# Optimization experiments

Hardware: AMD Instinct MI355X
Metric: run time of the kernel (lower is better)

## Reference

```python
import jax, jax.numpy as jnp
import numpy as np

# Static graph layout: B equal-size graphs of N nodes; first S nodes of each
# graph are 'sentence' nodes, the remaining N-S are 'other' nodes.
B, N, S, C = 64, 4096, 512, 128
TOTAL = B * N
E = 4_194_304          # avg degree 16
K_SENT = 3             # num_output_sentences
RATIO = 0.5
K_OTHER = int(np.ceil(RATIO * (N - S)))  # 1792 -> 1795 kept nodes per graph


def setup_inputs() -> dict:
    key = jax.random.key(0)
    k1, k2, k3 = jax.random.split(key, 3)
    x = jax.random.normal(k1, (TOTAL, C), dtype=jnp.float32)
    weight = jax.random.uniform(k2, (C,), dtype=jnp.float32)  # torch.rand(1, C)
    edge_index = jax.random.randint(k3, (2, E), 0, TOTAL, dtype=jnp.int32)
    batch = jnp.repeat(jnp.arange(B, dtype=jnp.int32), N)     # per-node graph id
    return {"x": x, "weight": weight, "edge_index": edge_index, "batch": batch}


def _pool(x, weight, edge_index, batch):
    # score_i = tanh(<x_i, w> / ||w||)   (min_score is None branch)
    score = jnp.tanh((x @ weight) / jnp.linalg.norm(weight))        # [TOTAL]
    score_b = score.reshape(B, N)

    # ragged-as-dense per-graph top-k (torch does dense reshape + sort + gather)
    base = (jnp.arange(B, dtype=jnp.int32) * N)[:, None]            # [B,1]
    _, sent_idx = jax.lax.top_k(score_b[:, :S], K_SENT)             # [B,K_SENT]
    _, other_idx = jax.lax.top_k(score_b[:, S:], K_OTHER)           # [B,K_OTHER]
    perm = jnp.concatenate([
        (sent_idx.astype(jnp.int32) + base).reshape(-1),            # all sentence picks first
        (other_idx.astype(jnp.int32) + S + base).reshape(-1),
    ])                                                              # [B*(K_SENT+K_OTHER)]

    x_out = x[perm] * score[perm][:, None]                          # multiplier == 1
    batch_out = batch[perm]

    # filter_adj: remap kept nodes to new ids; drop edges touching dropped nodes.
    node_map = jnp.full((TOTAL,), -1, dtype=jnp.int32).at[perm].set(
        jnp.arange(perm.shape[0], dtype=jnp.int32))
    row = node_map[edge_index[0]]
    col = node_map[edge_index[1]]
    keep = (row >= 0) & (col >= 0)
    # jit-friendly compaction: stable-sort kept edges to the front, pad tail with -1
    order = jnp.argsort(jnp.where(keep, 0, 1), stable=True)
    edge_index_new = jnp.stack([jnp.where(keep, row, -1)[order],
                                jnp.where(keep, col, -1)[order]])
    num_edges = keep.sum()
    return x_out, edge_index_new, batch_out, perm, score[perm], num_edges


def reference(x, weight, edge_index, batch):
    return _pool(x, weight, edge_index, batch)
```

## Files before the change

kernel.cpp:

```cpp
#include <hip/hip_runtime.h>
#include <hip/hip_bf16.h>
#include <stdint.h>

#define NB 64
#define NN 4096
#define NS 512
#define NC 128
#define NTOTAL (NB*NN)
#define NE 4194304
#define KSENT 3
#define KOTHER 1792
#define KPG (KSENT+KOTHER)
#define NP (NB*KPG)
#define NSENT_TOT (NB*KSENT)
#define NOTHER (NN-NS)

#define OFF_X     0ull
#define OFF_EDGE  14704640ull
#define OFF_BATCH 23093248ull
#define OFF_PERM  23208128ull
#define OFF_SCORE 23323008ull
#define OFF_NE    23437888ull

#define NEBLK 512
#define EPB   (NE/NEBLK)
#define STASH 2560
#define NGB   1024
#define NBW   (NTOTAL/32)

#define FLG_AGG (1ull<<62)
#define FLG_INC (2ull<<62)

__device__ float g_scores[NTOTAL];
__device__ int   g_perm[NP];
__device__ int   g_nodemap[NTOTAL];
__device__ uint32_t g_bits[NBW];
__device__ unsigned long long g_state[NEBLK];

__device__ __forceinline__ float bfr(float f){
  uint32_t u = __float_as_uint(f);
  uint32_t r = u + 0x7FFFu + ((u >> 16) & 1u);
  return __uint_as_float(r & 0xFFFF0000u);
}

__device__ __forceinline__ float xla_tanhf(float x){
#pragma clang fp contract(off)
  float xc = fminf(fmaxf(x, -7.90531110763549805f), 7.90531110763549805f);
  float x2 = __fmul_rn(xc, xc);
  float p = -2.76076847742355e-16f;
  p = __fadd_rn(__fmul_rn(p, x2),  2.00018790482477e-13f);
  p = __fadd_rn(__fmul_rn(p, x2), -8.60467152213735e-11f);
  p = __fadd_rn(__fmul_rn(p, x2),  5.12229709037114e-08f);
  p = __fadd_rn(__fmul_rn(p, x2),  1.48572235717979e-05f);
  p = __fadd_rn(__fmul_rn(p, x2),  6.37261928875436e-04f);
  p = __fadd_rn(__fmul_rn(p, x2),  4.89352455891786e-03f);
  p = __fmul_rn(xc, p);
  float q = 1.19825839466702e-06f;
  q = __fadd_rn(__fmul_rn(q, x2), 1.18534705686654e-04f);
  q = __fadd_rn(__fmul_rn(q, x2), 2.26843463243900e-03f);
  q = __fadd_rn(__fmul_rn(q, x2), 4.89352518554385e-03f);
  float r = __fdiv_rn(p, q);
  return (fabsf(x) < 0.0004f) ? x : r;
}

__global__ __launch_bounds__(256) void k_scores(const float* __restrict__ x,
                                                const float* __restrict__ w){
#pragma clang fp contract(off)
  int tid = threadIdx.x;
  int gid = blockIdx.x*256 + tid;
  if (gid < NTOTAL) g_nodemap[gid] = -1;
  if (blockIdx.x == 0){ g_state[tid] = 0ull; g_state[256+tid] = 0ull; }

  int grp = tid >> 4, j = tid & 15;
  int row = blockIdx.x*16 + grp;
  const float* rx = x + (size_t)row*NC;

  float wv[8];
#pragma unroll
  for (int k = 0; k < 8; ++k) wv[k] = w[k*16 + j];

  float an = 0.f, ad = 0.f;
#pragma unroll
  for (int k = 0; k < 8; ++k) an = __fadd_rn(an, __fmul_rn(wv[k], wv[k]));
#pragma unroll
  for (int k = 0; k < 8; ++k) ad = __fadd_rn(ad, __fmul_rn(rx[k*16 + j], wv[k]));

  float o;
  o = __shfl_down(an, 8); if (j < 8) an = __fadd_rn(an, o);
  o = __shfl_down(ad, 8); if (j < 8) ad = __fadd_rn(ad, o);
  o = __shfl_down(an, 4); if (j < 4) an = __fadd_rn(an, o);
  o = __shfl_down(ad, 4); if (j < 4) ad = __fadd_rn(ad, o);
  o = __shfl_down(an, 2); if (j < 2) an = __fadd_rn(an, o);
  o = __shfl_down(ad, 2); if (j < 2) ad = __fadd_rn(ad, o);
  o = __shfl_down(an, 1);
  float o2 = __shfl_down(ad, 1);
  if (j == 0){
    float nrm = __fsqrt_rn(__fadd_rn(an, o));
    float acc = __fadd_rn(ad, o2);
    float t = __fdiv_rn(acc, nrm);
    g_scores[row] = xla_tanhf(t);
  }
}

__device__ __forceinline__ unsigned long long skey(float s, int idx){
  uint32_t u = __float_as_uint(s);
  u = (u & 0x80000000u) ? ~u : (u | 0x80000000u);
  u = ~u;
  return ((unsigned long long)u << 32) | (uint32_t)idx;
}

__global__ __launch_bounds__(512) void k_topk(){
  __shared__ uint32_t keyA[NOTHER], keyB[NOTHER];
  __shared__ uint16_t idxA[NOTHER], idxB[NOTHER], rnk[NOTHER];
  __shared__ uint16_t cnt[8][256];
  __shared__ uint16_t tot[256], dbase[256];
  __shared__ unsigned long long smin[8];
  __shared__ unsigned long long swin;
  __shared__ uint32_t bl[NN/32];

  int g = blockIdx.x, tid = threadIdx.x;
  int lane = tid & 63, wv = tid >> 6;
  const float* sg = g_scores + g*NN;

  if (tid < NN/32) bl[tid] = 0u;
  __syncthreads();

  unsigned long long key = skey(sg[tid], tid);
  for (int t = 0; t < KSENT; ++t){
    unsigned long long v = key;
#pragma unroll
    for (int off = 32; off; off >>= 1){
      unsigned long long o = __shfl_down(v, off);
      v = (o < v) ? o : v;
    }
    if (lane == 0) smin[wv] = v;
    __syncthreads();
    if (tid == 0){
      unsigned long long mm = smin[0];
      for (int w2 = 1; w2 < 8; ++w2) if (smin[w2] < mm) mm = smin[w2];
      swin = mm;
    }
    __syncthreads();
    unsigned long long winner = swin;
    if (key == winner){
      int idx = (int)(winner & 0xFFFFFFFFull);
      int node = g*NN + idx, p = g*KSENT + t;
      g_perm[p] = node;
      g_nodemap[node] = p;
      atomicOr(&bl[idx >> 5], 1u << (idx & 31));
      key = ~0ull;
    }
    __syncthreads();
  }

  for (int i = tid; i < NOTHER; i += 512){
    uint32_t u = __float_as_uint(sg[NS + i]);
    u = (u & 0x80000000u) ? ~u : (u | 0x80000000u);
    keyA[i] = ~u;
    idxA[i] = (uint16_t)i;
  }
  __syncthreads();

  uint32_t* ksrc = keyA; uint32_t* kdst = keyB;
  uint16_t* isrc = idxA; uint16_t* idst = idxB;
  unsigned long long ltmask = (1ull << lane) - 1ull;
  int base = wv * 448;

  for (int pass = 0; pass < 4; ++pass){
    int shift = pass * 8;
    uint32_t* c32 = (uint32_t*)cnt[wv];
    c32[lane] = 0; c32[64 + lane] = 0;
    for (int r = 0; r < 7; ++r){
      int i = base + r*64 + lane;
      uint32_t k = ksrc[i];
      uint32_t d = (k >> shift) & 255u;
      unsigned long long m = ~0ull;
#pragma unroll
      for (int b = 0; b < 8; ++b){
        unsigned long long bb = __ballot((d >> b) & 1u);
        m &= ((d >> b) & 1u) ? bb : ~bb;
      }
      int rir = __popcll(m & ltmask);
      uint16_t bse = cnt[wv][d];
      rnk[i] = (uint16_t)(bse + rir);
      if ((m >> lane) == 1ull)
        cnt[wv][d] = (uint16_t)(bse + __popcll(m));
    }
    __syncthreads();
    if (tid < 256){
      int s = 0;
#pragma unroll
      for (int w2 = 0; w2 < 8; ++w2){
        int t2 = cnt[w2][tid]; cnt[w2][tid] = (uint16_t)s; s += t2;
      }
      tot[tid] = (uint16_t)s;
    }
    __syncthreads();
    if (tid < 64){
      int b4 = tid*4;
      int s0=tot[b4], s1=tot[b4+1], s2=tot[b4+2], s3=tot[b4+3];
      int lsum = s0+s1+s2+s3;
      int sc = lsum;
      for (int off = 1; off < 64; off <<= 1){
        int vv = __shfl_up(sc, off);
        if (lane >= off) sc += vv;
      }
      int excl = sc - lsum;
      dbase[b4]   = (uint16_t)excl;
      dbase[b4+1] = (uint16_t)(excl + s0);
      dbase[b4+2] = (uint16_t)(excl + s0 + s1);
      dbase[b4+3] = (uint16_t)(excl + s0 + s1 + s2);
    }
    __syncthreads();
    {
      int idx = tid;
#pragma unroll
      for (int kk = 0; kk < 4; ++kk){
        int w2 = (idx >> 8) & 7, d2 = idx & 255;
        cnt[w2][d2] = (uint16_t)(cnt[w2][d2] + dbase[d2]);
        idx += 512;
      }
    }
    __syncthreads();
    for (int r = 0; r < 7; ++r){
      int i = base + r*64 + lane;
      uint32_t k = ksrc[i];
      uint32_t d = (k >> shift) & 255u;
      int dest = cnt[wv][d] + rnk[i];
      kdst[dest] = k; idst[dest] = isrc[i];
    }
    __syncthreads();
    uint32_t* tk = ksrc; ksrc = kdst; kdst = tk;
    uint16_t* ti = isrc; isrc = idst; idst = ti;
  }
  for (int j = tid; j < KOTHER; j += 512){
    int li = NS + (int)isrc[j];
    int node = g*NN + li;
    int p = NSENT_TOT + g*KOTHER + j;
    g_perm[p] = node;
    g_nodemap[node] = p;
    atomicOr(&bl[li >> 5], 1u << (li & 31));
  }
  __syncthreads();
  if (tid < NN/32) g_bits[g*(NN/32) + tid] = bl[tid];
}

__global__ __launch_bounds__(512) void k2(const int* __restrict__ ei,
                                          const float* __restrict__ x,
                                          float* __restrict__ out){
  __shared__ uint32_t bm[NBW];
  __shared__ int2 rc[STASH];
  __shared__ int wsum[8];
  __shared__ int s_off;
  int b = blockIdx.x, tid = threadIdx.x;

  if (b >= NEBLK){
    const size_t total4 = (size_t)NP*NC/4;
    for (size_t q = (size_t)(b - NEBLK)*512 + tid; q < total4;
         q += (size_t)NGB*512){
      int p  = (int)(q >> 5);
      int c4 = (int)(q & 31);
      int node = g_perm[p];
      float s = g_scores[node];
      float4 v = *(const float4*)(x + (size_t)node*NC + c4*4);
      float4 o;
      o.x = bfr(__fmul_rn(v.x, s));
      o.y = bfr(__fmul_rn(v.y, s));
      o.z = bfr(__fmul_rn(v.z, s));
      o.w = bfr(__fmul_rn(v.w, s));
      *(float4*)(out + OFF_X + (size_t)p*NC + c4*4) = o;
      if (c4 == 0){
        out[OFF_BATCH + p] = bfr((float)(node >> 12));
        out[OFF_PERM  + p] = bfr((float)node);
        out[OFF_SCORE + p] = bfr(s);
      }
    }
    return;
  }

  int lane = tid & 63, wid = tid >> 6;
  int base = b * EPB;
  unsigned long long ltm = (1ull << lane) - 1ull;

  {
    uint4* d4 = (uint4*)bm;
    const uint4* s4 = (const uint4*)g_bits;
#pragma unroll
    for (int kk = 0; kk < 4; ++kk) d4[tid + kk*512] = s4[tid + kk*512];
  }
  if (tid == 0) s_off = 0;
  __syncthreads();

  int running = 0;
  for (int s = 0; s < EPB; s += 512){
    int e = base + s + tid;
    int u = ei[e], v = ei[NE + e];
    bool keep = ((bm[u >> 5] >> (u & 31)) & 1u) &&
                ((bm[v >> 5] >> (v & 31)) & 1u);
    unsigned long long m = __ballot(keep);
    if (lane == 0) wsum[wid] = __popcll(m);
    __syncthreads();
    int wbase = 0;
#pragma unroll
    for (int w2 = 0; w2 < 8; ++w2) if (w2 < wid) wbase += wsum[w2];
    int tot = 0;
#pragma unroll
    for (int w2 = 0; w2 < 8; ++w2) tot += wsum[w2];
    if (keep){
      int lp = running + wbase + __popcll(m & ltm);
      if (lp < STASH){
        int2 p; p.x = g_nodemap[u]; p.y = g_nodemap[v]; rc[lp] = p;
      }
    }
    running += tot;
    __syncthreads();
  }
  int myc = running;

  if (b == 0){
    if (tid == 0)
      atomicExch(&g_state[0], FLG_INC | (unsigned long long)(uint32_t)myc);
  } else if (wid == 0){
    if (lane == 0)
      atomicExch(&g_state[b], FLG_AGG | (unsigned long long)(uint32_t)myc);
    int prev = 0, win = b - 1;
    bool done = false;
    while (!done){
      int idxl = win - lane;
      unsigned long long st = (idxl >= 0) ? atomicAdd(&g_state[idxl], 0ull)
                                          : FLG_INC;
      unsigned f = (unsigned)(st >> 62);
      unsigned long long readym = __ballot(f != 0u);
      unsigned long long incm   = __ballot(f == 2u);
      if (incm){
        int l0 = __ffsll((long long)incm) - 1;
        unsigned long long needm = (l0 == 63) ? ~0ull : ((1ull << (l0+1)) - 1ull);
        if ((readym & needm) == needm){
          int contrib = (lane <= l0) ? (int)(uint32_t)st : 0;
#pragma unroll
          for (int off = 32; off; off >>= 1)
            contrib += __shfl_down(contrib, off);
          if (lane == 0) prev += contrib;
          done = true;
        }
      } else if (readym == ~0ull){
        int contrib = (int)(uint32_t)st;
#pragma unroll
        for (int off = 32; off; off >>= 1)
          contrib += __shfl_down(contrib, off);
        if (lane == 0) prev += contrib;
        win -= 64;
      } else {
        __builtin_amdgcn_s_sleep(2);
      }
    }
    if (lane == 0){
      atomicExch(&g_state[b], FLG_INC | (unsigned long long)(uint32_t)(prev + myc));
      s_off = prev;
      if (b == NEBLK-1)
        out[OFF_NE] = bfr((float)(prev + myc));
    }
  }
  __syncthreads();
  int off = s_off;

  int lim = myc < STASH ? myc : STASH;
  for (int i = tid; i < lim; i += 512){
    int2 p = rc[i];
    out[OFF_EDGE + off + i]      = bfr((float)p.x);
    out[OFF_EDGE + NE + off + i] = bfr((float)p.y);
  }
  if (myc > STASH){
    running = 0;
    __syncthreads();
    for (int s = 0; s < EPB; s += 512){
      int e = base + s + tid;
      int u = ei[e], v = ei[NE + e];
      bool keep = ((bm[u >> 5] >> (u & 31)) & 1u) &&
                  ((bm[v >> 5] >> (v & 31)) & 1u);
      unsigned long long m = __ballot(keep);
      if (lane == 0) wsum[wid] = __popcll(m);
      __syncthreads();
      int wbase = 0;
#pragma unroll
      for (int w2 = 0; w2 < 8; ++w2) if (w2 < wid) wbase += wsum[w2];
      int tot = 0;
#pragma unroll
      for (int w2 = 0; w2 < 8; ++w2) tot += wsum[w2];
      if (keep){
        int lp = running + wbase + __popcll(m & ltm);
        if (lp >= STASH){
          out[OFF_EDGE + off + lp]      = bfr((float)g_nodemap[u]);
          out[OFF_EDGE + NE + off + lp] = bfr((float)g_nodemap[v]);
        }
      }
      running += tot;
      __syncthreads();
    }
  }

  int drops = EPB - myc;
  int dropoff = base - off;
  int t0 = NE - dropoff - drops;
  for (int i = tid; i < drops; i += 512){
    out[OFF_EDGE + t0 + i]      = -1.0f;
    out[OFF_EDGE + NE + t0 + i] = -1.0f;
  }
}

extern "C" void kernel_launch(void* const* d_in, const int* in_sizes, int n_in,
                              void* d_out, int out_size, void* d_ws, size_t ws_size,
                              hipStream_t stream) {
  const float* x = (const float*)d_in[0];
  const float* w = (const float*)d_in[1];
  const int*   ei = (const int*)d_in[2];
  float* out = (float*)d_out;

  hipLaunchKernelGGL(k_scores, dim3(NTOTAL/16),   dim3(256), 0, stream, x, w);
  hipLaunchKernelGGL(k_topk,   dim3(NB),          dim3(512), 0, stream);
  hipLaunchKernelGGL(k2,       dim3(NEBLK + NGB), dim3(512), 0, stream, ei, x, out);
}
```

Before: 90.98 us.

## Compact edges with per-thread 16-edge bitmasks instead of per-iteration block ballots

Each thread now loads 16 contiguous edges with vector loads and builds a keep bitmask. A single wavefront scan plus a block-level sum replaces the 16 iterations of ballot, shared-memory sum and two barriers. The shared-memory stash and the overflow second pass are removed, and kept edges are re-read from global memory and written directly at their scanned positions. This cuts barriers and LDS use, which may raise occupancy. In exchange, writes are no longer coalesced across threads because each thread writes its own contiguous run, and the edge reads are repeated.

```diff
diff --git a/kernel.cpp b/kernel.cpp
--- a/kernel.cpp
+++ b/kernel.cpp
@@ -24,7 +24,6 @@
 
 #define NEBLK 512
 #define EPB   (NE/NEBLK)
-#define STASH 2560
 #define NGB   1024
 #define NBW   (NTOTAL/32)
 
@@ -249,7 +248,6 @@
                                           const float* __restrict__ x,
                                           float* __restrict__ out){
   __shared__ uint32_t bm[NBW];
-  __shared__ int2 rc[STASH];
   __shared__ int wsum[8];
   __shared__ int s_off;
   int b = blockIdx.x, tid = threadIdx.x;
@@ -280,7 +278,7 @@
 
   int lane = tid & 63, wid = tid >> 6;
   int base = b * EPB;
-  unsigned long long ltm = (1ull << lane) - 1ull;
+  int e0 = base + tid*16;
 
   {
     uint4* d4 = (uint4*)bm;
@@ -291,31 +289,37 @@
   if (tid == 0) s_off = 0;
   __syncthreads();
 
-  int running = 0;
-  for (int s = 0; s < EPB; s += 512){
-    int e = base + s + tid;
-    int u = ei[e], v = ei[NE + e];
-    bool keep = ((bm[u >> 5] >> (u & 31)) & 1u) &&
-                ((bm[v >> 5] >> (v & 31)) & 1u);
-    unsigned long long m = __ballot(keep);
-    if (lane == 0) wsum[wid] = __popcll(m);
-    __syncthreads();
-    int wbase = 0;
-#pragma unroll
-    for (int w2 = 0; w2 < 8; ++w2) if (w2 < wid) wbase += wsum[w2];
-    int tot = 0;
-#pragma unroll
-    for (int w2 = 0; w2 < 8; ++w2) tot += wsum[w2];
-    if (keep){
-      int lp = running + wbase + __popcll(m & ltm);
-      if (lp < STASH){
-        int2 p; p.x = g_nodemap[u]; p.y = g_nodemap[v]; rc[lp] = p;
-      }
-    }
-    running += tot;
-    __syncthreads();
-  }
-  int myc = running;
+  uint32_t mask = 0;
+  {
+    const uint4* r0 = (const uint4*)(ei + e0);
+    const uint4* r1 = (const uint4*)(ei + (size_t)NE + e0);
+#pragma unroll
+    for (int k = 0; k < 4; ++k){
+      uint4 uu = r0[k], vv = r1[k];
+      uint32_t b0 = (bm[uu.x>>5] >> (uu.x&31)) & (bm[vv.x>>5] >> (vv.x&31)) & 1u;
+      uint32_t b1 = (bm[uu.y>>5] >> (uu.y&31)) & (bm[vv.y>>5] >> (vv.y&31)) & 1u;
+      uint32_t b2 = (bm[uu.z>>5] >> (uu.z&31)) & (bm[vv.z>>5] >> (vv.z&31)) & 1u;
+      uint32_t b3 = (bm[uu.w>>5] >> (uu.w&31)) & (bm[vv.w>>5] >> (vv.w&31)) & 1u;
+      mask |= (b0 | (b1<<1) | (b2<<2) | (b3<<3)) << (k*4);
+    }
+  }
+  int c = __popc(mask);
+
+  int sc = c;
+  for (int off = 1; off < 64; off <<= 1){
+    int v = __shfl_up(sc, off);
+    if (lane >= off) sc += v;
+  }
+  if (lane == 63) wsum[wid] = sc;
+  __syncthreads();
+  int wbase = 0, myc = 0;
+#pragma unroll
+  for (int w2 = 0; w2 < 8; ++w2){
+    int t2 = wsum[w2];
+    if (w2 < wid) wbase += t2;
+    myc += t2;
+  }
+  int myoff = wbase + sc - c;
 
   if (b == 0){
     if (tid == 0)
@@ -364,38 +368,16 @@
   __syncthreads();
   int off = s_off;
 
-  int lim = myc < STASH ? myc : STASH;
-  for (int i = tid; i < lim; i += 512){
-    int2 p = rc[i];
-    out[OFF_EDGE + off + i]      = bfr((float)p.x);
-    out[OFF_EDGE + NE + off + i] = bfr((float)p.y);
-  }
-  if (myc > STASH){
-    running = 0;
-    __syncthreads();
-    for (int s = 0; s < EPB; s += 512){
-      int e = base + s + tid;
-      int u = ei[e], v = ei[NE + e];
-      bool keep = ((bm[u >> 5] >> (u & 31)) & 1u) &&
-                  ((bm[v >> 5] >> (v & 31)) & 1u);
-      unsigned long long m = __ballot(keep);
-      if (lane == 0) wsum[wid] = __popcll(m);
-      __syncthreads();
-      int wbase = 0;
-#pragma unroll
-      for (int w2 = 0; w2 < 8; ++w2) if (w2 < wid) wbase += wsum[w2];
-      int tot = 0;
-#pragma unroll
-      for (int w2 = 0; w2 < 8; ++w2) tot += wsum[w2];
-      if (keep){
-        int lp = running + wbase + __popcll(m & ltm);
-        if (lp >= STASH){
-          out[OFF_EDGE + off + lp]      = bfr((float)g_nodemap[u]);
-          out[OFF_EDGE + NE + off + lp] = bfr((float)g_nodemap[v]);
-        }
-      }
-      running += tot;
-      __syncthreads();
+  {
+    int pos = off + myoff;
+    uint32_t mm = mask;
+    while (mm){
+      int k = __ffs(mm) - 1; mm &= mm - 1;
+      int e = e0 + k;
+      int u = ei[e], v = ei[(size_t)NE + e];
+      out[OFF_EDGE + pos]      = bfr((float)g_nodemap[u]);
+      out[OFF_EDGE + NE + pos] = bfr((float)g_nodemap[v]);
+      ++pos;
     }
   }
 
```

Result: slower. 104.7 us (+15.1%).

## Batch edge-keep compaction into one pass with a single barrier and vectorized fill

Applied to the files above, without the earlier changes.

The edge filter loop now loads all 16 edge chunks per thread up front, packs the keep bits into a register, runs the ballots, and stores per-wave counts for every chunk in shared memory. A single barrier then lets each thread compute its prefix offsets locally, replacing the two barriers per chunk that were used before. The overflow path reuses the stored counts instead of recomputing the keep test, and the -1 padding for dropped edges is written with float4 stores. In exchange, register use goes up and edge indices are re-read from global memory for kept edges.

```diff
diff --git a/kernel.cpp b/kernel.cpp
--- a/kernel.cpp
+++ b/kernel.cpp
@@ -250,7 +250,7 @@
                                           float* __restrict__ out){
   __shared__ uint32_t bm[NBW];
   __shared__ int2 rc[STASH];
-  __shared__ int wsum[8];
+  __shared__ int wcnt[128];
   __shared__ int s_off;
   int b = blockIdx.x, tid = threadIdx.x;
 
@@ -291,31 +291,46 @@
   if (tid == 0) s_off = 0;
   __syncthreads();
 
-  int running = 0;
-  for (int s = 0; s < EPB; s += 512){
-    int e = base + s + tid;
-    int u = ei[e], v = ei[NE + e];
-    bool keep = ((bm[u >> 5] >> (u & 31)) & 1u) &&
-                ((bm[v >> 5] >> (v & 31)) & 1u);
-    unsigned long long m = __ballot(keep);
-    if (lane == 0) wsum[wid] = __popcll(m);
-    __syncthreads();
-    int wbase = 0;
-#pragma unroll
-    for (int w2 = 0; w2 < 8; ++w2) if (w2 < wid) wbase += wsum[w2];
-    int tot = 0;
-#pragma unroll
-    for (int w2 = 0; w2 < 8; ++w2) tot += wsum[w2];
-    if (keep){
-      int lp = running + wbase + __popcll(m & ltm);
-      if (lp < STASH){
-        int2 p; p.x = g_nodemap[u]; p.y = g_nodemap[v]; rc[lp] = p;
-      }
-    }
-    running += tot;
-    __syncthreads();
-  }
-  int myc = running;
+  uint32_t keep16 = 0;
+#pragma unroll
+  for (int s = 0; s < 16; ++s){
+    int e = base + s*512 + tid;
+    uint32_t u = (uint32_t)ei[e], v = (uint32_t)ei[(size_t)NE + e];
+    keep16 |= (((bm[u>>5] >> (u&31)) & (bm[v>>5] >> (v&31)) & 1u) << s);
+  }
+  uint32_t lpack[4] = {0,0,0,0};
+#pragma unroll
+  for (int s = 0; s < 16; ++s){
+    unsigned long long m = __ballot((keep16 >> s) & 1u);
+    lpack[s>>2] |= ((uint32_t)__popcll(m & ltm)) << ((s&3)*8);
+    if (lane == 0) wcnt[s*8 + wid] = __popcll(m);
+  }
+  __syncthreads();
+
+  int run = 0;
+#pragma unroll
+  for (int s = 0; s < 16; ++s){
+    int wb = 0, tot = 0;
+#pragma unroll
+    for (int w2 = 0; w2 < 8; ++w2){
+      int t2 = wcnt[s*8 + w2];
+      wb += (w2 < wid) ? t2 : 0;
+      tot += t2;
+    }
+    if ((keep16 >> s) & 1u){
+      int lp = (int)((lpack[s>>2] >> ((s&3)*8)) & 255u);
+      int posL = run + wb + lp;
+      if (posL < STASH){
+        int e = base + s*512 + tid;
+        int2 p;
+        p.x = g_nodemap[ei[e]];
+        p.y = g_nodemap[ei[(size_t)NE + e]];
+        rc[posL] = p;
+      }
+    }
+    run += tot;
+  }
+  int myc = run;
 
   if (b == 0){
     if (tid == 0)
@@ -371,40 +386,45 @@
     out[OFF_EDGE + NE + off + i] = bfr((float)p.y);
   }
   if (myc > STASH){
-    running = 0;
-    __syncthreads();
-    for (int s = 0; s < EPB; s += 512){
-      int e = base + s + tid;
-      int u = ei[e], v = ei[NE + e];
-      bool keep = ((bm[u >> 5] >> (u & 31)) & 1u) &&
-                  ((bm[v >> 5] >> (v & 31)) & 1u);
-      unsigned long long m = __ballot(keep);
-      if (lane == 0) wsum[wid] = __popcll(m);
-      __syncthreads();
-      int wbase = 0;
-#pragma unroll
-      for (int w2 = 0; w2 < 8; ++w2) if (w2 < wid) wbase += wsum[w2];
-      int tot = 0;
-#pragma unroll
-      for (int w2 = 0; w2 < 8; ++w2) tot += wsum[w2];
-      if (keep){
-        int lp = running + wbase + __popcll(m & ltm);
-        if (lp >= STASH){
-          out[OFF_EDGE + off + lp]      = bfr((float)g_nodemap[u]);
-          out[OFF_EDGE + NE + off + lp] = bfr((float)g_nodemap[v]);
+    int run2 = 0;
+#pragma unroll
+    for (int s = 0; s < 16; ++s){
+      int wb = 0, tot = 0;
+#pragma unroll
+      for (int w2 = 0; w2 < 8; ++w2){
+        int t2 = wcnt[s*8 + w2];
+        wb += (w2 < wid) ? t2 : 0;
+        tot += t2;
+      }
+      if ((keep16 >> s) & 1u){
+        int lp = (int)((lpack[s>>2] >> ((s&3)*8)) & 255u);
+        int posL = run2 + wb + lp;
+        if (posL >= STASH){
+          int e = base + s*512 + tid;
+          out[OFF_EDGE + off + posL]      = bfr((float)g_nodemap[ei[e]]);
+          out[OFF_EDGE + NE + off + posL] = bfr((float)g_nodemap[ei[(size_t)NE + e]]);
         }
       }
-      running += tot;
-      __syncthreads();
+      run2 += tot;
     }
   }
 
   int drops = EPB - myc;
   int dropoff = base - off;
-  int t0 = NE - dropoff - drops;
-  for (int i = tid; i < drops; i += 512){
-    out[OFF_EDGE + t0 + i]      = -1.0f;
-    out[OFF_EDGE + NE + t0 + i] = -1.0f;
+  size_t t0 = (size_t)(NE - dropoff - drops);
+  float4 mv4; mv4.x = mv4.y = mv4.z = mv4.w = -1.0f;
+#pragma unroll
+  for (int r2 = 0; r2 < 2; ++r2){
+    size_t st = OFF_EDGE + (size_t)r2*NE + t0;
+    int head = (int)((4 - (st & 3)) & 3);
+    if (head > drops) head = drops;
+    for (int i = tid; i < head; i += 512) out[st + i] = -1.0f;
+    int nv = (drops - head) >> 2;
+    float4* p4 = (float4*)(out + st + head);
+    for (int i = tid; i < nv; i += 512) p4[i] = mv4;
+    int rem = drops - head - (nv << 2);
+    size_t rbase = st + head + ((size_t)nv << 2);
+    for (int i = tid; i < rem; i += 512) out[rbase + i] = -1.0f;
   }
 }
 
```

Result: slower. 93.60 us (+2.9%).
